# Kernel optimization log

Hardware: AMD Instinct MI355X
Metric: run time of the kernel (lower is better)

## Reference

```python
import jax, jax.numpy as jnp
import numpy as np

NCE_T = 0.07   # opt.nce_T
EPS = 1e-8     # torch CosineSimilarity eps
DIAG_FILL = -10.0

N, D = 8192, 256

def setup_inputs() -> dict:
    key = jax.random.key(0)
    kq, kk = jax.random.split(key)
    feat_q = jax.random.normal(kq, (N, D), dtype=jnp.float32)
    feat_k = jax.random.normal(kk, (N, D), dtype=jnp.float32)
    return {"feat_q": feat_q, "feat_k": feat_k}

def reference(feat_q, feat_k):
    # feat_k is detached in the original
    feat_k = jax.lax.stop_gradient(feat_k)
    nq = jnp.linalg.norm(feat_q, axis=-1)            # [N]
    nk = jnp.linalg.norm(feat_k, axis=-1)            # [N]
    # positive cosine similarity (paired rows)
    l_pos = jnp.sum(feat_q * feat_k, axis=-1) / jnp.maximum(nq * nk, EPS)  # [N]
    # full N x N cosine similarity via GEMM (torch does a broadcasted version)
    sim = (feat_q @ feat_k.T) / jnp.maximum(nq[:, None] * nk[None, :], EPS)  # [N,N]
    # mask self-similarities with -10.0 BEFORE dividing by temperature
    diag = jnp.eye(sim.shape[0], dtype=bool)
    l_neg = jnp.where(diag, DIAG_FILL, sim)
    out = jnp.concatenate([l_pos[:, None], l_neg], axis=1) / NCE_T  # [N, N+1]
    # cross-entropy vs target class 0, reduction='none'
    loss = jax.scipy.special.logsumexp(out, axis=1) - out[:, 0]     # [N]
    return loss
```

## Files before the change

### kernel.cpp

```cpp
#include <hip/hip_runtime.h>
#include <stdint.h>
#include <math.h>

#define NROWS 8192
#define DDIM  256
#define BM    128
#define BN    128
#define GJ    8
#define COLS_PER_GROUP (NROWS / GJ)

constexpr float INV_T  = 1.0f / 0.07f;
constexpr float LOG2E  = 1.44269504f;
constexpr float K1     = INV_T * LOG2E;

typedef __bf16 bf16x8 __attribute__((ext_vector_type(8)));
typedef float  f32x4  __attribute__((ext_vector_type(4)));

__device__ __forceinline__ void async_copy16(const uint16_t* g, uint16_t* l) {
    __builtin_amdgcn_global_load_lds(
        (const __attribute__((address_space(1))) uint32_t*)g,
        (__attribute__((address_space(3))) uint32_t*)l, 16, 0, 0);
}

__device__ inline uint16_t f2bf(float f) {
    uint32_t u = __float_as_uint(f);
    u += 0x7fffu + ((u >> 16) & 1u);
    return (uint16_t)(u >> 16);
}

__global__ __launch_bounds__(256) void norm_convert_kernel(
    const float* __restrict__ fq, const float* __restrict__ fk,
    uint16_t* __restrict__ qb, uint16_t* __restrict__ kb,
    float* __restrict__ lpT)
{
    const int wave = threadIdx.x >> 6;
    const int lane = threadIdx.x & 63;
    const int row  = blockIdx.x * 4 + wave;

    if (row < NROWS) {
        const float* qsrc = fq + (size_t)row * DDIM;
        const float* ksrc = fk + (size_t)row * DDIM;
        float4 vq = ((const float4*)qsrc)[lane];
        float4 vk = ((const float4*)ksrc)[lane];
        float ssq = vq.x*vq.x + vq.y*vq.y + vq.z*vq.z + vq.w*vq.w;
        float ssk = vk.x*vk.x + vk.y*vk.y + vk.z*vk.z + vk.w*vk.w;
        float dqk = vq.x*vk.x + vq.y*vk.y + vq.z*vk.z + vq.w*vk.w;
        #pragma unroll
        for (int m = 1; m < 64; m <<= 1) {
            ssq += __shfl_xor(ssq, m, 64);
            ssk += __shfl_xor(ssk, m, 64);
            dqk += __shfl_xor(dqk, m, 64);
        }
        float r = rsqrtf(ssq);
        ushort4 o;
        o.x = f2bf(vq.x * r); o.y = f2bf(vq.y * r); o.z = f2bf(vq.z * r); o.w = f2bf(vq.w * r);
        ((ushort4*)(qb + (size_t)row * DDIM))[lane] = o;
        if (lane == 0) {
            float denom = fmaxf(sqrtf(ssq) * sqrtf(ssk), 1e-8f);
            lpT[row] = (dqk / denom) * INV_T;
        }
    } else {
        const int r_ = row - NROWS;
        const float* src = fk + (size_t)r_ * DDIM;
        float4 v = ((const float4*)src)[lane];
        float ss = v.x*v.x + v.y*v.y + v.z*v.z + v.w*v.w;
        #pragma unroll
        for (int m = 1; m < 64; m <<= 1) ss += __shfl_xor(ss, m, 64);
        float r = rsqrtf(ss);
        ushort4 o;
        o.x = f2bf(v.x * r); o.y = f2bf(v.y * r); o.z = f2bf(v.z * r); o.w = f2bf(v.w * r);
        ((ushort4*)(kb + (size_t)r_ * DDIM))[lane] = o;
    }
}

__global__ __launch_bounds__(256, 2) void nce_main_kernel(
    const uint16_t* __restrict__ qb, const uint16_t* __restrict__ kb,
    float* __restrict__ gpl)
{
    __shared__ __align__(16) uint16_t lds_q[BM * DDIM];
    __shared__ __align__(16) uint16_t lds_k[2 * BN * 32];

    const int tid    = threadIdx.x;
    const int wave   = tid >> 6;
    const int lane   = tid & 63;
    const int quad   = lane >> 4;
    const int lanelo = lane & 15;
    const int wr     = wave >> 1;
    const int wc     = wave & 1;
    const int rowBase      = blockIdx.x * BM;
    const int colGroupBase = blockIdx.y * COLS_PER_GROUP;

    #pragma unroll
    for (int i = 0; i < 16; ++i) {
        int S   = (wave * 16 + i) * 64 + lane;
        int row = S >> 5;
        int ch  = (S & 31) ^ (row & 31);
        async_copy16(qb + (size_t)(rowBase + row) * DDIM + ch * 8,
                     lds_q + (size_t)(wave * 16 + i) * 512);
    }

    int kS0   = wave * 128 + lane;
    int krow0 = kS0 >> 2;
    int kch0  = (lane & 3) ^ ((krow0 >> 1) & 3);
    int krow1 = (kS0 + 64) >> 2;
    int kch1  = (lane & 3) ^ ((krow1 >> 1) & 3);
    const uint16_t* kbase0 = kb + (size_t)(colGroupBase + krow0) * DDIM + kch0 * 8;
    const uint16_t* kbase1 = kb + (size_t)(colGroupBase + krow1) * DDIM + kch1 * 8;
    uint16_t* kl0 = lds_k + wave * 1024;

    async_copy16(kbase0, kl0);
    async_copy16(kbase1, kl0 + 512);

    uint4 gset[4][2];
    #pragma unroll
    for (int n = 1; n <= 4; ++n) {
        const int off = (n & 7) << 5;
        gset[n & 3][0] = *(const uint4*)(kbase0 + off);
        gset[n & 3][1] = *(const uint4*)(kbase1 + off);
    }

    __syncthreads();

    int rq[4], rq31[4];
    #pragma unroll
    for (int mt = 0; mt < 4; ++mt) {
        rq[mt]   = wr * 64 + mt * 16 + lanelo;
        rq31[mt] = rq[mt] & 31;
    }
    int bvoff[4];
    #pragma unroll
    for (int nt = 0; nt < 4; ++nt) {
        int rk = wc * 64 + nt * 16 + lanelo;
        bvoff[nt] = rk * 32 + (quad ^ ((lanelo >> 1) & 3)) * 8;
    }
    const int wbase = wave * 1024 + lane * 8;

    float l_run[16];
    #pragma unroll
    for (int i = 0; i < 16; ++i) l_run[i] = 0.f;

    for (int jt = 0; jt < 8; ++jt) {
        f32x4 acc[4][4];
        #pragma unroll
        for (int mt = 0; mt < 4; ++mt)
            #pragma unroll
            for (int nt = 0; nt < 4; ++nt)
                acc[mt][nt] = (f32x4){0.f, 0.f, 0.f, 0.f};

        #pragma unroll
        for (int kk = 0; kk < 8; ++kk) {
            const int p    = (jt << 3) + kk;
            const int buf  = p & 1;
            const int nbuf = buf ^ 1;
            const int s    = (kk + 1) & 3;

            bf16x8 av[4], bv[4];
            #pragma unroll
            for (int mt = 0; mt < 4; ++mt) {
                int chp = ((kk << 2) + quad) ^ rq31[mt];
                av[mt] = *(const bf16x8*)&lds_q[rq[mt] * 256 + chp * 8];
            }
            #pragma unroll
            for (int nt = 0; nt < 4; ++nt)
                bv[nt] = *(const bf16x8*)&lds_k[buf * 4096 + bvoff[nt]];

            {
                uint16_t* wp = lds_k + nbuf * 4096 + wbase;
                *(uint4*)wp         = gset[s][0];
                *(uint4*)(wp + 512) = gset[s][1];
            }
            {
                const int np  = (p + 5) & 63;
                const int off = ((np >> 3) << 15) + ((np & 7) << 5);
                gset[s][0] = *(const uint4*)(kbase0 + off);
                gset[s][1] = *(const uint4*)(kbase1 + off);
            }

            #pragma unroll
            for (int mt = 0; mt < 4; ++mt)
                #pragma unroll
                for (int nt = 0; nt < 4; ++nt)
                    acc[mt][nt] = __builtin_amdgcn_mfma_f32_16x16x32_bf16(av[mt], bv[nt], acc[mt][nt], 0, 0, 0);

            asm volatile("s_waitcnt lgkmcnt(0)" ::: "memory");
            asm volatile("s_barrier" ::: "memory");
        }

        #pragma unroll
        for (int mt = 0; mt < 4; ++mt) {
            #pragma unroll
            for (int rg = 0; rg < 4; ++rg) {
                float s = 0.f;
                #pragma unroll
                for (int nt = 0; nt < 4; ++nt)
                    s += exp2f(fmaf(acc[mt][nt][rg], K1, -K1));
                l_run[mt * 4 + rg] += s;
            }
        }
    }

    #pragma unroll
    for (int i = 0; i < 16; ++i) {
        float v = l_run[i];
        v += __shfl_xor(v, 1, 64);
        v += __shfl_xor(v, 2, 64);
        v += __shfl_xor(v, 4, 64);
        v += __shfl_xor(v, 8, 64);
        l_run[i] = v;
    }
    __syncthreads();

    float* pl = (float*)lds_k;
    if (lanelo == 0) {
        #pragma unroll
        for (int mt = 0; mt < 4; ++mt)
            #pragma unroll
            for (int rg = 0; rg < 4; ++rg) {
                int lr = wr * 64 + mt * 16 + quad * 4 + rg;
                pl[wc * 128 + lr] = l_run[mt * 4 + rg];
            }
    }
    __syncthreads();
    if (tid < 128) {
        float L = pl[tid] + pl[128 + tid];
        gpl[(size_t)blockIdx.y * NROWS + rowBase + tid] = L;
    }
}

__global__ __launch_bounds__(256) void finalize_kernel(
    const float* __restrict__ gpl, const float* __restrict__ lpT,
    float* __restrict__ out)
{
    int t = blockIdx.x * 256 + threadIdx.x;
    if (t >= NROWS) return;
    float L = 0.f;
    #pragma unroll
    for (int g = 0; g < GJ; ++g) L += gpl[g * NROWS + t];
    out[t] = INV_T + __logf(L) - lpT[t];
}

extern "C" void kernel_launch(void* const* d_in, const int* in_sizes, int n_in,
                              void* d_out, int out_size, void* d_ws, size_t ws_size,
                              hipStream_t stream) {
    const float* fq = (const float*)d_in[0];
    const float* fk = (const float*)d_in[1];
    char* ws = (char*)d_ws;
    uint16_t* qb  = (uint16_t*)(ws);
    uint16_t* kb  = (uint16_t*)(ws + 4194304);
    float*    lpT = (float*)(ws + 8388608);
    float*    gpl = (float*)(ws + 8421376);

    norm_convert_kernel<<<(2 * NROWS) / 4, 256, 0, stream>>>(fq, fk, qb, kb, lpT);
    dim3 grid(NROWS / BM, GJ);
    nce_main_kernel<<<grid, 256, 0, stream>>>(qb, kb, gpl);
    finalize_kernel<<<NROWS / 256, 256, 0, stream>>>(gpl, lpT, (float*)d_out);
}
```

Measured before the change: 125.5 us.

## Give each wave private K tiles loaded async to drop per-step block barriers

Reorganizes the main GEMM so each wave owns a private 32-column slice of K, covers all 128 Q rows, and streams its own K chunks into a private double-buffered LDS region using global_load_lds. This removes the per-k-step s_barrier and the register-staged prefetch that passed through VGPRs, replacing them with per-wave vmcnt waits. In exchange each wave reads all 8 A fragments from LDS per step (more LDS read traffic per MFMA), and the final reduction now combines four wave partials.

```diff
diff --git a/kernel.cpp b/kernel.cpp
--- a/kernel.cpp
+++ b/kernel.cpp
@@ -78,15 +78,13 @@
     float* __restrict__ gpl)
 {
     __shared__ __align__(16) uint16_t lds_q[BM * DDIM];
-    __shared__ __align__(16) uint16_t lds_k[2 * BN * 32];
+    __shared__ __align__(16) uint16_t lds_k[8192];
 
     const int tid    = threadIdx.x;
     const int wave   = tid >> 6;
     const int lane   = tid & 63;
     const int quad   = lane >> 4;
     const int lanelo = lane & 15;
-    const int wr     = wave >> 1;
-    const int wc     = wave & 1;
     const int rowBase      = blockIdx.x * BM;
     const int colGroupBase = blockIdx.y * COLS_PER_GROUP;
 
@@ -99,108 +97,82 @@
                      lds_q + (size_t)(wave * 16 + i) * 512);
     }
 
-    int kS0   = wave * 128 + lane;
-    int krow0 = kS0 >> 2;
-    int kch0  = (lane & 3) ^ ((krow0 >> 1) & 3);
-    int krow1 = (kS0 + 64) >> 2;
-    int kch1  = (lane & 3) ^ ((krow1 >> 1) & 3);
-    const uint16_t* kbase0 = kb + (size_t)(colGroupBase + krow0) * DDIM + kch0 * 8;
-    const uint16_t* kbase1 = kb + (size_t)(colGroupBase + krow1) * DDIM + kch1 * 8;
-    uint16_t* kl0 = lds_k + wave * 1024;
-
-    async_copy16(kbase0, kl0);
-    async_copy16(kbase1, kl0 + 512);
-
-    uint4 gset[4][2];
-    #pragma unroll
-    for (int n = 1; n <= 4; ++n) {
-        const int off = (n & 7) << 5;
-        gset[n & 3][0] = *(const uint4*)(kbase0 + off);
-        gset[n & 3][1] = *(const uint4*)(kbase1 + off);
-    }
+    const int c0 = (lane & 3) ^ ((lane >> 3) & 3);
+    const uint16_t* kpb0 = kb + (size_t)(colGroupBase + wave * 32 +      (lane >> 2)) * DDIM + c0 * 8;
+    const uint16_t* kpb1 = kb + (size_t)(colGroupBase + wave * 32 + 16 + (lane >> 2)) * DDIM + c0 * 8;
+    uint16_t* kw = lds_k + wave * 2048;
+
+    async_copy16(kpb0,      kw);
+    async_copy16(kpb1,      kw + 512);
+    async_copy16(kpb0 + 32, kw + 1024);
+    async_copy16(kpb1 + 32, kw + 1536);
 
     __syncthreads();
 
-    int rq[4], rq31[4];
-    #pragma unroll
-    for (int mt = 0; mt < 4; ++mt) {
-        rq[mt]   = wr * 64 + mt * 16 + lanelo;
-        rq31[mt] = rq[mt] & 31;
-    }
-    int bvoff[4];
-    #pragma unroll
-    for (int nt = 0; nt < 4; ++nt) {
-        int rk = wc * 64 + nt * 16 + lanelo;
-        bvoff[nt] = rk * 32 + (quad ^ ((lanelo >> 1) & 3)) * 8;
-    }
-    const int wbase = wave * 1024 + lane * 8;
-
-    float l_run[16];
-    #pragma unroll
-    for (int i = 0; i < 16; ++i) l_run[i] = 0.f;
+    int bvoff[2];
+    #pragma unroll
+    for (int nt = 0; nt < 2; ++nt)
+        bvoff[nt] = (nt * 16 + lanelo) * 32 + (quad ^ ((lanelo >> 1) & 3)) * 8;
+
+    float l_run[32];
+    #pragma unroll
+    for (int i = 0; i < 32; ++i) l_run[i] = 0.f;
 
     for (int jt = 0; jt < 8; ++jt) {
-        f32x4 acc[4][4];
-        #pragma unroll
-        for (int mt = 0; mt < 4; ++mt)
-            #pragma unroll
-            for (int nt = 0; nt < 4; ++nt)
+        f32x4 acc[8][2];
+        #pragma unroll
+        for (int mt = 0; mt < 8; ++mt)
+            #pragma unroll
+            for (int nt = 0; nt < 2; ++nt)
                 acc[mt][nt] = (f32x4){0.f, 0.f, 0.f, 0.f};
 
         #pragma unroll
         for (int kk = 0; kk < 8; ++kk) {
-            const int p    = (jt << 3) + kk;
-            const int buf  = p & 1;
-            const int nbuf = buf ^ 1;
-            const int s    = (kk + 1) & 3;
-
-            bf16x8 av[4], bv[4];
-            #pragma unroll
-            for (int mt = 0; mt < 4; ++mt) {
-                int chp = ((kk << 2) + quad) ^ rq31[mt];
-                av[mt] = *(const bf16x8*)&lds_q[rq[mt] * 256 + chp * 8];
+            const int p = (jt << 3) + kk;
+
+            asm volatile("s_waitcnt vmcnt(2)" ::: "memory");
+
+            bf16x8 av[8], bv[2];
+            #pragma unroll
+            for (int mt = 0; mt < 8; ++mt) {
+                int rq  = mt * 16 + lanelo;
+                int chp = ((kk << 2) + quad) ^ (lanelo + ((mt & 1) << 4));
+                av[mt] = *(const bf16x8*)&lds_q[rq * 256 + chp * 8];
             }
-            #pragma unroll
-            for (int nt = 0; nt < 4; ++nt)
-                bv[nt] = *(const bf16x8*)&lds_k[buf * 4096 + bvoff[nt]];
-
+            const int bufo = (p & 1) << 10;
+            bv[0] = *(const bf16x8*)&lds_k[wave * 2048 + bufo + bvoff[0]];
+            bv[1] = *(const bf16x8*)&lds_k[wave * 2048 + bufo + bvoff[1]];
+
+            asm volatile("s_waitcnt lgkmcnt(0)" ::: "memory");
             {
-                uint16_t* wp = lds_k + nbuf * 4096 + wbase;
-                *(uint4*)wp         = gset[s][0];
-                *(uint4*)(wp + 512) = gset[s][1];
+                const int np  = (p + 2) & 63;
+                const int off = ((np >> 3) << 15) + ((np & 7) << 5);
+                async_copy16(kpb0 + off, kw + bufo);
+                async_copy16(kpb1 + off, kw + bufo + 512);
             }
-            {
-                const int np  = (p + 5) & 63;
-                const int off = ((np >> 3) << 15) + ((np & 7) << 5);
-                gset[s][0] = *(const uint4*)(kbase0 + off);
-                gset[s][1] = *(const uint4*)(kbase1 + off);
-            }
-
-            #pragma unroll
-            for (int mt = 0; mt < 4; ++mt)
+            __builtin_amdgcn_sched_barrier(0);
+
+            #pragma unroll
+            for (int mt = 0; mt < 8; ++mt)
                 #pragma unroll
-                for (int nt = 0; nt < 4; ++nt)
-                    acc[mt][nt] = __builtin_amdgcn_mfma_f32_16x16x32_bf16(av[mt], bv[nt], acc[mt][nt], 0, 0, 0);
-
-            asm volatile("s_waitcnt lgkmcnt(0)" ::: "memory");
-            asm volatile("s_barrier" ::: "memory");
-        }
-
-        #pragma unroll
-        for (int mt = 0; mt < 4; ++mt) {
+                for (int nt = 0; nt < 2; ++nt)
+                    acc[mt][nt] = __builtin_amdgcn_mfma_f32_16x16x32_bf16(
+                        av[mt], bv[nt], acc[mt][nt], 0, 0, 0);
+        }
+
+        #pragma unroll
+        for (int mt = 0; mt < 8; ++mt) {
             #pragma unroll
             for (int rg = 0; rg < 4; ++rg) {
-                float s = 0.f;
-                #pragma unroll
-                for (int nt = 0; nt < 4; ++nt)
-                    s += exp2f(fmaf(acc[mt][nt][rg], K1, -K1));
+                float s = exp2f(fmaf(acc[mt][0][rg], K1, -K1))
+                        + exp2f(fmaf(acc[mt][1][rg], K1, -K1));
                 l_run[mt * 4 + rg] += s;
             }
         }
     }
 
     #pragma unroll
-    for (int i = 0; i < 16; ++i) {
+    for (int i = 0; i < 32; ++i) {
         float v = l_run[i];
         v += __shfl_xor(v, 1, 64);
         v += __shfl_xor(v, 2, 64);
@@ -208,21 +180,20 @@
         v += __shfl_xor(v, 8, 64);
         l_run[i] = v;
     }
+
     __syncthreads();
 
     float* pl = (float*)lds_k;
     if (lanelo == 0) {
         #pragma unroll
-        for (int mt = 0; mt < 4; ++mt)
-            #pragma unroll
-            for (int rg = 0; rg < 4; ++rg) {
-                int lr = wr * 64 + mt * 16 + quad * 4 + rg;
-                pl[wc * 128 + lr] = l_run[mt * 4 + rg];
-            }
+        for (int mt = 0; mt < 8; ++mt)
+            #pragma unroll
+            for (int rg = 0; rg < 4; ++rg)
+                pl[wave * 128 + mt * 16 + quad * 4 + rg] = l_run[mt * 4 + rg];
     }
     __syncthreads();
     if (tid < 128) {
-        float L = pl[tid] + pl[128 + tid];
+        float L = pl[tid] + pl[128 + tid] + pl[256 + tid] + pl[384 + tid];
         gpl[(size_t)blockIdx.y * NROWS + rowBase + tid] = L;
     }
 }
```

Measured after the change: 105.6 us. -15.8%, faster.
